# Performance work log

Measured on AMD Instinct MI355X. Metric: run time of the kernel, lower is better.

## Reference

```python
import jax, jax.numpy as jnp
import numpy as np

N, D, H, ED, E, T, L = 100000, 128, 128, 64, 500000, 2, 4


def _ln(x, g, b):
    m = jnp.mean(x, axis=-1, keepdims=True)
    v = jnp.var(x, axis=-1, keepdims=True)
    return (x - m) * jax.lax.rsqrt(v + 1e-5) * g + b


def _seg_softmax(s, seg, n):
    # softmax over edges grouped by segment id (torch scatter-softmax)
    m = jax.ops.segment_max(s, seg, num_segments=n)
    m = jnp.where(jnp.isfinite(m), m, 0.0)
    e = jnp.exp(s - m[seg])
    z = jax.ops.segment_sum(e, seg, num_segments=n)
    return e / (z[seg] + 1e-16)


def setup_inputs() -> dict:
    key = jax.random.key(0)
    ks = iter(jax.random.split(key, 64))
    p = lambda shape: jax.random.normal(next(ks), shape, dtype=jnp.float32) * 0.05
    inp = {
        'node_features': jax.random.normal(next(ks), (N, D), dtype=jnp.float32),
        'edge_features': jax.random.normal(next(ks), (T, E, ED), dtype=jnp.float32),
        'node_levels': jax.random.randint(next(ks), (N,), 0, L, dtype=jnp.int32),
        'edge_index': jax.random.randint(next(ks), (T, 2, E), 0, N, dtype=jnp.int32),
        # NodeLevelAttention params (stacked over T edge types)
        'nl_node_W': p((T, D, H)), 'nl_node_b': p((T, H)),
        'nl_edge_W': p((T, ED, H)), 'nl_edge_b': p((T, H)),
        'nl_att_W1': p((T, 3 * H, H)), 'nl_att_b1': p((T, H)),
        'nl_att_W2': p((T, H, 1)), 'nl_att_b2': p((T, 1)),
        'nl_out_W': p((T, H, H)), 'nl_out_b': p((T, H)),
        'nl_ln_g': jnp.ones((T, H), jnp.float32), 'nl_ln_b': jnp.zeros((T, H), jnp.float32),
        # EdgeLevelAttention params
        'el_att_W1': p((T, H, H)), 'el_att_b1': p((T, H)),
        'el_att_W2': p((T, H, 1)), 'el_att_b2': p((T, 1)),
        'el_out_W': p((H, H)), 'el_out_b': p((H,)),
        'el_ln_g': jnp.ones((H,), jnp.float32), 'el_ln_b': jnp.zeros((H,), jnp.float32),
        # HierarchicalAwarenessModule params
        'hl_proj_W': p((L, H, H)), 'hl_proj_b': p((L, H)),
        'hi_att_W1': p((2 * H, H)), 'hi_att_b1': p((H,)),
        'hi_att_W2': p((H, 1)), 'hi_att_b2': p((1,)),
        'hl_out_W': p((H, H)), 'hl_out_b': p((H,)),
        'hl_ln_g': jnp.ones((H,), jnp.float32), 'hl_ln_b': jnp.zeros((H,), jnp.float32),
    }
    return inp


def reference(node_features, edge_features, node_levels, edge_index,
              nl_node_W, nl_node_b, nl_edge_W, nl_edge_b,
              nl_att_W1, nl_att_b1, nl_att_W2, nl_att_b2,
              nl_out_W, nl_out_b, nl_ln_g, nl_ln_b,
              el_att_W1, el_att_b1, el_att_W2, el_att_b2,
              el_out_W, el_out_b, el_ln_g, el_ln_b,
              hl_proj_W, hl_proj_b, hi_att_W1, hi_att_b1,
              hi_att_W2, hi_att_b2, hl_out_W, hl_out_b, hl_ln_g, hl_ln_b):
    embs, scores = [], []
    for t in range(T):  # small fixed set of edge types
        h = node_features @ nl_node_W[t] + nl_node_b[t]              # [N,H]
        he = edge_features[t] @ nl_edge_W[t] + nl_edge_b[t]          # [E,H]
        s, d = edge_index[t, 0], edge_index[t, 1]
        cat = jnp.concatenate([h[s], h[d], he], axis=-1)             # [E,3H]
        a = jnp.tanh(cat @ nl_att_W1[t] + nl_att_b1[t]) @ nl_att_W2[t] + nl_att_b2[t]
        alpha = _seg_softmax(a[:, 0], s, N)[:, None]                 # softmax over out-edges of src
        agg = jax.ops.segment_sum(alpha * h[d], s, num_segments=N)  # [N,H]
        emb = jax.nn.relu(_ln(agg @ nl_out_W[t] + nl_out_b[t], nl_ln_g[t], nl_ln_b[t]))
        embs.append(emb)
        scores.append(jnp.tanh(emb @ el_att_W1[t] + el_att_b1[t]) @ el_att_W2[t] + el_att_b2[t])
    # EdgeLevelAttention: softmax over edge types per node
    w = jax.nn.softmax(jnp.concatenate(scores, axis=1), axis=1)      # [N,T]
    fused = sum(embs[t] * w[:, t:t + 1] for t in range(T))
    fused = jax.nn.relu(_ln(fused @ el_out_W + el_out_b, el_ln_g, el_ln_b))
    # HierarchicalAwarenessModule (vectorized form of the per-node loop)
    proj_all = jnp.einsum('nd,ldh->lnh', fused, hl_proj_W) + hl_proj_b[:, None, :]
    hf = proj_all[node_levels, jnp.arange(N)]                        # [N,H] level-specific projection
    counts = jax.ops.segment_sum(jnp.ones((N,), fused.dtype), node_levels, num_segments=L)
    lmean = jax.ops.segment_sum(hf, node_levels, num_segments=L) / jnp.maximum(counts, 1.0)[:, None]
    W1a, W1b = hi_att_W1[:H], hi_att_W1[H:]                          # split concat([h_i, mean_l]) matmul
    sc = jnp.tanh((hf @ W1a)[:, None, :] + (lmean @ W1b)[None, :, :] + hi_att_b1) @ hi_att_W2 + hi_att_b2
    aw = jax.nn.softmax(sc[..., 0], axis=1)                          # [N,L]
    enhanced = aw @ lmean                                            # [N,H]
    return jax.nn.relu(_ln(enhanced @ hl_out_W + hl_out_b, hl_ln_g, hl_ln_b))
```

## Files before the change

### kernel.cpp

```cpp
#include <hip/hip_runtime.h>
#include <math.h>

#define NN 100000
#define EE 500000

typedef __attribute__((ext_vector_type(8))) short bf16x8;
typedef __attribute__((ext_vector_type(4))) float f32x4;
#define MFMA __builtin_amdgcn_mfma_f32_16x16x32_bf16

__device__ inline short f2bf(float x) {
    union { float f; unsigned u; } v; v.f = x;
    unsigned r = v.u + 0x7FFF + ((v.u >> 16) & 1);
    return (short)(r >> 16);
}
__device__ inline float bf2f(unsigned short h) {
    union { unsigned u; float f; } v; v.u = ((unsigned)h) << 16; return v.f;
}
__device__ inline float tanhf_fast(float x) {
    float e = __expf(2.0f * x);
    return 1.0f - 2.0f * __builtin_amdgcn_rcpf(e + 1.0f);
}

__device__ inline bf16x8 mk_hi(const float* p) {
    float4 a = *(const float4*)p, b = *(const float4*)(p + 4);
    float v[8] = {a.x, a.y, a.z, a.w, b.x, b.y, b.z, b.w};
    bf16x8 h;
#pragma unroll
    for (int i = 0; i < 8; i++) h[i] = f2bf(v[i]);
    return h;
}
__device__ inline void mk_split(const float* p, bf16x8& hi, bf16x8& lo) {
    float4 a = *(const float4*)p, b = *(const float4*)(p + 4);
    float v[8] = {a.x, a.y, a.z, a.w, b.x, b.y, b.z, b.w};
#pragma unroll
    for (int i = 0; i < 8; i++) {
        short h = f2bf(v[i]);
        hi[i] = h;
        lo[i] = f2bf(v[i] - bf2f((unsigned short)h));
    }
}

__global__ void k_zero(float* __restrict__ p, size_t n) {
    size_t i = (size_t)blockIdx.x * blockDim.x + threadIdx.x;
    size_t stride = (size_t)gridDim.x * blockDim.x;
    for (; i < n; i += stride) p[i] = 0.0f;
}
__global__ void k_zeroi(int* __restrict__ p, int n) {
    int i = blockIdx.x * blockDim.x + threadIdx.x;
    if (i < n) p[i] = 0;
}

__global__ __launch_bounds__(256) void k_hist(const int* __restrict__ eis, int* __restrict__ deg) {
    int e = blockIdx.x * 256 + threadIdx.x;
    if (e < EE) atomicAdd(&deg[eis[e]], 1);
}
__global__ __launch_bounds__(512) void k_scan1(const int* __restrict__ deg,
                                               int* __restrict__ tmp, int* __restrict__ bsum) {
    __shared__ int sh[2][512];
    int b = blockIdx.x, tid = threadIdx.x;
    int i = b * 512 + tid;
    int v = (i < NN) ? deg[i] : 0;
    int cur = 0;
    sh[0][tid] = v;
    __syncthreads();
    for (int off = 1; off < 512; off <<= 1) {
        int nxt = cur ^ 1;
        int a = sh[cur][tid];
        if (tid >= off) a += sh[cur][tid - off];
        sh[nxt][tid] = a;
        __syncthreads();
        cur = nxt;
    }
    int incl = sh[cur][tid];
    if (i < NN) tmp[i] = incl;
    if (tid == 511) bsum[b] = incl;
}
__global__ void k_scan2(const int* __restrict__ bsum, int* __restrict__ boff) {
    __shared__ int sh[2][256];
    int tid = threadIdx.x;
    int v = (tid < 196) ? bsum[tid] : 0;
    int cur = 0;
    sh[0][tid] = v;
    __syncthreads();
    for (int off = 1; off < 256; off <<= 1) {
        int nxt = cur ^ 1;
        int a = sh[cur][tid];
        if (tid >= off) a += sh[cur][tid - off];
        sh[nxt][tid] = a;
        __syncthreads();
        cur = nxt;
    }
    boff[tid] = sh[cur][tid] - v;
}
__global__ __launch_bounds__(512) void k_scan3(const int* __restrict__ deg,
                                               const int* __restrict__ tmp,
                                               const int* __restrict__ boff,
                                               int* __restrict__ rowptr, int* __restrict__ cursor) {
    int i = blockIdx.x * 512 + threadIdx.x;
    if (i < NN) {
        int r = tmp[i] - deg[i] + boff[blockIdx.x];
        rowptr[i] = r;
        cursor[i] = r;
    }
    if (i == 0) rowptr[NN] = EE;
}
__global__ __launch_bounds__(256) void k_csr_scatter(const int* __restrict__ eis,
                                                     const int* __restrict__ eid,
                                                     int* __restrict__ cursor,
                                                     int* __restrict__ epos,
                                                     int* __restrict__ cdst) {
    int e = blockIdx.x * 256 + threadIdx.x;
    if (e < EE) {
        int s = eis[e];
        int p = atomicAdd(&cursor[s], 1);
        epos[e] = p;
        cdst[p] = eid[e];
    }
}

__global__ __launch_bounds__(256) void k_count(const int* __restrict__ lev, int* __restrict__ cnt4) {
    __shared__ int lc[4];
    int tid = threadIdx.x;
    if (tid < 4) lc[tid] = 0;
    __syncthreads();
    for (long n = (long)blockIdx.x * 256 + tid; n < NN; n += (long)gridDim.x * 256)
        atomicAdd(&lc[lev[n]], 1);
    __syncthreads();
    if (tid < 4 && lc[tid]) atomicAdd(&cnt4[tid], lc[tid]);
}

__global__ void k_scan(const int* __restrict__ cnt4, int* __restrict__ off4,
                       int* __restrict__ boff5, int* __restrict__ cursor) {
    int o = 0, b = 0;
    for (int l = 0; l < 4; l++) {
        off4[l] = o; cursor[l] = o; boff5[l] = b;
        o += cnt4[l];
        b += (cnt4[l] + 15) >> 4;
    }
    boff5[4] = b;
}

__global__ __launch_bounds__(256) void k_scatter(const int* __restrict__ lev,
                                                 int* __restrict__ cursor,
                                                 int* __restrict__ perm) {
    __shared__ int lc[4], lb[4], lc2[4];
    int tid = threadIdx.x;
    if (tid < 4) { lc[tid] = 0; lc2[tid] = 0; }
    __syncthreads();
    int start = blockIdx.x * 800, end = start + 800;
    if (end > NN) end = NN;
    for (int n = start + tid; n < end; n += 256) atomicAdd(&lc[lev[n]], 1);
    __syncthreads();
    if (tid < 4 && lc[tid]) lb[tid] = atomicAdd(&cursor[tid], lc[tid]);
    __syncthreads();
    for (int n = start + tid; n < end; n += 256) {
        int l = lev[n];
        int p = atomicAdd(&lc2[l], 1);
        perm[lb[l] + p] = n;
    }
}

__global__ void k_prep_head(const float* __restrict__ Wn, const float* __restrict__ bn,
                            const float* __restrict__ W1, const float* __restrict__ b1,
                            const float* __restrict__ We, const float* __restrict__ be,
                            unsigned short* __restrict__ WhT, unsigned short* __restrict__ WUT,
                            unsigned short* __restrict__ WVT, unsigned short* __restrict__ WET,
                            float* __restrict__ beff) {
    __shared__ float red[2];
    int j = blockIdx.x, k = threadIdx.x;
    WhT[j * 128 + k] = (unsigned short)f2bf(Wn[k * 128 + j]);
    float su = 0.0f, sv = 0.0f;
    for (int m = 0; m < 128; m++) {
        float wkm = Wn[k * 128 + m];
        su = fmaf(wkm, W1[m * 128 + j], su);
        sv = fmaf(wkm, W1[(128 + m) * 128 + j], sv);
    }
    WUT[j * 128 + k] = (unsigned short)f2bf(su);
    WVT[j * 128 + k] = (unsigned short)f2bf(sv);
    if (k < 64) {
        float se = 0.0f;
        for (int m = 0; m < 128; m++) se = fmaf(We[k * 128 + m], W1[(256 + m) * 128 + j], se);
        WET[j * 64 + k] = (unsigned short)f2bf(se);
    }
    float tk = bn[k] * (W1[k * 128 + j] + W1[(128 + k) * 128 + j]) + be[k] * W1[(256 + k) * 128 + j];
#pragma unroll
    for (int o = 32; o > 0; o >>= 1) tk += __shfl_down(tk, o);
    if ((k & 63) == 0) red[k >> 6] = tk;
    __syncthreads();
    if (k == 0) beff[j] = b1[j] + red[0] + red[1];
}

struct WSrc { const float* s[6]; };
__global__ void k_prep_tail(WSrc ps, unsigned short* __restrict__ hi,
                            unsigned short* __restrict__ lo) {
    int m = blockIdx.x >> 6, blk = blockIdx.x & 63;
    const float* src = ps.s[m];
    unsigned short* h = hi + (size_t)m * 16384;
    unsigned short* l = lo + (size_t)m * 16384;
    int idx = blk * 256 + threadIdx.x;
    int k = idx >> 7, j = idx & 127;
    float v = src[idx];
    short hh = f2bf(v);
    h[j * 128 + k] = (unsigned short)hh;
    l[j * 128 + k] = (unsigned short)f2bf(v - bf2f((unsigned short)hh));
}

__global__ void k_prep_q(const float* __restrict__ hpW, const float* __restrict__ hpb,
                         const float* __restrict__ hW1a,
                         unsigned short* __restrict__ QWhi, unsigned short* __restrict__ QWlo,
                         float* __restrict__ qb) {
    int gidx = blockIdx.x * 256 + threadIdx.x;
    if (gidx < 4 * 16384) {
        int l = gidx >> 14, rem = gidx & 16383;
        int k = rem >> 7, j = rem & 127;
        const float* wr = hpW + (size_t)l * 16384 + (size_t)k * 128;
        float v = 0.0f;
        for (int m = 0; m < 128; m++) v = fmaf(wr[m], hW1a[m * 128 + j], v);
        short hh = f2bf(v);
        QWhi[(size_t)l * 16384 + j * 128 + k] = (unsigned short)hh;
        QWlo[(size_t)l * 16384 + j * 128 + k] = (unsigned short)f2bf(v - bf2f((unsigned short)hh));
    } else {
        int e = gidx - 4 * 16384;
        if (e < 512) {
            int l = e >> 7, j = e & 127;
            float v = 0.0f;
            for (int m = 0; m < 128; m++) v = fmaf(hpb[l * 128 + m], hW1a[m * 128 + j], v);
            qb[l * 128 + j] = v;
        }
    }
}

__global__ __launch_bounds__(256) void k_head(const float* __restrict__ nf,
                                              const unsigned short* __restrict__ WhT,
                                              const unsigned short* __restrict__ WUT,
                                              const unsigned short* __restrict__ WVT,
                                              const float* __restrict__ bn,
                                              unsigned short* __restrict__ hbf,
                                              unsigned short* __restrict__ U,
                                              unsigned short* __restrict__ V) {
    __shared__ __align__(16) float T[16][132];
    int tid = threadIdx.x;
    long row0 = (long)blockIdx.x * 16;
#pragma unroll
    for (int i = 0; i < 8; i++) {
        int idx = tid + i * 256;
        int r = idx >> 7, c = idx & 127;
        T[r][c] = nf[(row0 + r) * 128 + c];
    }
    __syncthreads();
    int w = tid >> 6, lane = tid & 63, lr = lane & 15, lg = lane >> 4;
    bf16x8 A[4];
#pragma unroll
    for (int k = 0; k < 4; k++) A[k] = mk_hi(&T[lr][k * 32 + lg * 8]);
    int col0 = w * 32 + lr, col1 = col0 + 16;
#pragma unroll
    for (int o = 0; o < 3; o++) {
        const unsigned short* wb = (o == 0) ? WhT : (o == 1) ? WUT : WVT;
        unsigned short* ob = (o == 0) ? hbf : (o == 1) ? U : V;
        const unsigned short* w0 = wb + (size_t)col0 * 128 + lg * 8;
        const unsigned short* w1 = wb + (size_t)col1 * 128 + lg * 8;
        f32x4 a0 = {0.f, 0.f, 0.f, 0.f}, a1 = {0.f, 0.f, 0.f, 0.f};
#pragma unroll
        for (int k = 0; k < 4; k++) {
            a0 = MFMA(A[k], *(const bf16x8*)(w0 + k * 32), a0, 0, 0, 0);
            a1 = MFMA(A[k], *(const bf16x8*)(w1 + k * 32), a1, 0, 0, 0);
        }
        float bb0 = (o == 0) ? bn[col0] : 0.0f;
        float bb1 = (o == 0) ? bn[col1] : 0.0f;
        unsigned short* op = ob + (size_t)row0 * 128;
#pragma unroll
        for (int i = 0; i < 4; i++) {
            int r = lg * 4 + i;
            op[(size_t)r * 128 + col0] = (unsigned short)f2bf(a0[i] + bb0);
            op[(size_t)r * 128 + col1] = (unsigned short)f2bf(a1[i] + bb1);
        }
    }
}

__global__ __launch_bounds__(256) void k_edge3(const float* __restrict__ ef,
                                               const int* __restrict__ eis,
                                               const int* __restrict__ eid,
                                               const int* __restrict__ epos,
                                               const unsigned short* __restrict__ WET,
                                               const unsigned short* __restrict__ U,
                                               const unsigned short* __restrict__ V,
                                               const float* __restrict__ beff,
                                               const float* __restrict__ W2,
                                               const float* __restrict__ b2p,
                                               float* __restrict__ ebuf) {
    __shared__ __align__(16) float pre[64][132];
    __shared__ float part[4][64];
    int tid = threadIdx.x, w = tid >> 6, lane = tid & 63, lr = lane & 15, lg = lane >> 4;
    long e0 = (long)blockIdx.x * 64;
    long remE = (long)EE - e0;
    int nE = remE < 64 ? (int)remE : 64;
    int n16 = (nE + 15) >> 4;
    {
        int eL = tid >> 2;
        int c4 = tid & 3;
        if (eL < nE) {
            long e = e0 + eL;
            int s = eis[e], d = eid[e];
            const unsigned short* up = U + (size_t)s * 128 + c4 * 32;
            const unsigned short* vp = V + (size_t)d * 128 + c4 * 32;
#pragma unroll
            for (int i = 0; i < 4; i++) {
                bf16x8 uv = *(const bf16x8*)(up + i * 8);
                bf16x8 vv = *(const bf16x8*)(vp + i * 8);
                float4 lo4, hi4;
                lo4.x = bf2f((unsigned short)uv[0]) + bf2f((unsigned short)vv[0]);
                lo4.y = bf2f((unsigned short)uv[1]) + bf2f((unsigned short)vv[1]);
                lo4.z = bf2f((unsigned short)uv[2]) + bf2f((unsigned short)vv[2]);
                lo4.w = bf2f((unsigned short)uv[3]) + bf2f((unsigned short)vv[3]);
                hi4.x = bf2f((unsigned short)uv[4]) + bf2f((unsigned short)vv[4]);
                hi4.y = bf2f((unsigned short)uv[5]) + bf2f((unsigned short)vv[5]);
                hi4.z = bf2f((unsigned short)uv[6]) + bf2f((unsigned short)vv[6]);
                hi4.w = bf2f((unsigned short)uv[7]) + bf2f((unsigned short)vv[7]);
                *(float4*)&pre[eL][c4 * 32 + i * 8] = lo4;
                *(float4*)&pre[eL][c4 * 32 + i * 8 + 4] = hi4;
            }
        }
    }
    int col0 = w * 32 + lr, col1 = col0 + 16;
    bf16x8 B0[2], B1[2];
#pragma unroll
    for (int kk = 0; kk < 2; kk++) {
        B0[kk] = *(const bf16x8*)(WET + (size_t)col0 * 64 + kk * 32 + lg * 8);
        B1[kk] = *(const bf16x8*)(WET + (size_t)col1 * 64 + kk * 32 + lg * 8);
    }
    float be0 = beff[col0], be1 = beff[col1], w20 = W2[col0], w21 = W2[col1];
    __syncthreads();
    for (int i16 = 0; i16 < n16; i16++) {
        long eg0 = e0 + i16 * 16;
        const float* ep = ef + (size_t)(eg0 + lr) * 64;
        f32x4 a0 = {0.f, 0.f, 0.f, 0.f}, a1 = {0.f, 0.f, 0.f, 0.f};
#pragma unroll
        for (int kk = 0; kk < 2; kk++) {
            bf16x8 a = mk_hi(ep + kk * 32 + lg * 8);
            a0 = MFMA(a, B0[kk], a0, 0, 0, 0);
            a1 = MFMA(a, B1[kk], a1, 0, 0, 0);
        }
#pragma unroll
        for (int i = 0; i < 4; i++) {
            int eL = i16 * 16 + lg * 4 + i;
            float v = tanhf_fast(a0[i] + pre[eL][col0] + be0) * w20 +
                      tanhf_fast(a1[i] + pre[eL][col1] + be1) * w21;
            v += __shfl_xor(v, 1);
            v += __shfl_xor(v, 2);
            v += __shfl_xor(v, 4);
            v += __shfl_xor(v, 8);
            if (lr == 0) part[w][eL] = v;
        }
    }
    __syncthreads();
    if (tid < nE) {
        long e = e0 + tid;
        float a = part[0][tid] + part[1][tid] + part[2][tid] + part[3][tid] + b2p[0];
        ebuf[epos[e]] = __expf(a);
    }
}

__global__ __launch_bounds__(256) void k_tailA2(const int* __restrict__ rowptr,
                                                const int* __restrict__ cdst,
                                                const float* __restrict__ ebufC,
                                                const unsigned short* __restrict__ hbf,
                                                const unsigned short* __restrict__ Whi,
                                                const unsigned short* __restrict__ Wlo,
                                                const float* __restrict__ ob,
                                                const float* __restrict__ g,
                                                const float* __restrict__ bln,
                                                const unsigned short* __restrict__ Shi,
                                                const float* __restrict__ sb1,
                                                const float* __restrict__ sW2,
                                                const float* __restrict__ sb2,
                                                float* __restrict__ emb,
                                                float* __restrict__ scores, int t) {
    __shared__ __align__(16) float T[16][132];
    __shared__ __align__(16) float T2[16][132];
    __shared__ float mu16[16], rs16[16], part[4][16];
    int tid = threadIdx.x;
    long row0 = (long)blockIdx.x * 16;
    {
        int r16 = tid >> 4, sub = tid & 15;
        long n = row0 + r16;
        int p0 = rowptr[n], p1 = rowptr[n + 1];
        float acc[8] = {0, 0, 0, 0, 0, 0, 0, 0};
        float sev = 0.0f;
        for (int p = p0; p < p1; p++) {
            int d = cdst[p];
            float ev = ebufC[p];
            bf16x8 hv = *(const bf16x8*)(hbf + (size_t)d * 128 + sub * 8);
            sev += ev;
#pragma unroll
            for (int i = 0; i < 8; i++) acc[i] = fmaf(ev, bf2f((unsigned short)hv[i]), acc[i]);
        }
        float inv = 1.0f / (sev + 1e-16f);
#pragma unroll
        for (int i = 0; i < 8; i++) T[r16][sub * 8 + i] = acc[i] * inv;
    }
    __syncthreads();
    int w = tid >> 6, lane = tid & 63, lr = lane & 15, lg = lane >> 4;
    int col0 = w * 32 + lr, col1 = col0 + 16;
    int j = tid & 127, half = tid >> 7;
    {
        bf16x8 ahi[4], alo[4];
#pragma unroll
        for (int k = 0; k < 4; k++) mk_split(&T[lr][k * 32 + lg * 8], ahi[k], alo[k]);
        const unsigned short* wh0 = Whi + (size_t)col0 * 128 + lg * 8;
        const unsigned short* wl0 = Wlo + (size_t)col0 * 128 + lg * 8;
        const unsigned short* wh1 = Whi + (size_t)col1 * 128 + lg * 8;
        const unsigned short* wl1 = Wlo + (size_t)col1 * 128 + lg * 8;
        f32x4 a0 = {0.f, 0.f, 0.f, 0.f}, a1 = {0.f, 0.f, 0.f, 0.f};
#pragma unroll
        for (int k = 0; k < 4; k++) {
            bf16x8 bh = *(const bf16x8*)(wh0 + k * 32), bl = *(const bf16x8*)(wl0 + k * 32);
            a0 = MFMA(ahi[k], bh, a0, 0, 0, 0);
            a0 = MFMA(alo[k], bh, a0, 0, 0, 0);
            a0 = MFMA(ahi[k], bl, a0, 0, 0, 0);
            bh = *(const bf16x8*)(wh1 + k * 32); bl = *(const bf16x8*)(wl1 + k * 32);
            a1 = MFMA(ahi[k], bh, a1, 0, 0, 0);
            a1 = MFMA(alo[k], bh, a1, 0, 0, 0);
            a1 = MFMA(ahi[k], bl, a1, 0, 0, 0);
        }
#pragma unroll
        for (int i = 0; i < 4; i++) {
            int r = lg * 4 + i;
            T2[r][col0] = a0[i] + ob[col0];
            T2[r][col1] = a1[i] + ob[col1];
        }
    }
    __syncthreads();
    {
        int gr = tid >> 4, l16 = tid & 15;
        float sm = 0.0f, sq = 0.0f;
#pragma unroll
        for (int i = 0; i < 8; i++) {
            float v = T2[gr][l16 + 16 * i];
            sm += v; sq += v * v;
        }
#pragma unroll
        for (int m = 1; m < 16; m <<= 1) { sm += __shfl_xor(sm, m); sq += __shfl_xor(sq, m); }
        if (l16 == 0) {
            float mean = sm * (1.0f / 128.0f);
            float var = sq * (1.0f / 128.0f) - mean * mean;
            mu16[gr] = mean;
            rs16[gr] = rsqrtf(var + 1e-5f);
        }
    }
    __syncthreads();
    {
        float gj = g[j], bb = bln[j];
#pragma unroll
        for (int r = 0; r < 8; r++) {
            int rr = half * 8 + r;
            float v = fmaxf((T2[rr][j] - mu16[rr]) * rs16[rr] * gj + bb, 0.0f);
            emb[(row0 + rr) * 128 + j] = v;
            T2[rr][j] = v;
        }
    }
    __syncthreads();
    {
        bf16x8 ah[4];
#pragma unroll
        for (int k = 0; k < 4; k++) ah[k] = mk_hi(&T2[lr][k * 32 + lg * 8]);
        const unsigned short* wh0 = Shi + (size_t)col0 * 128 + lg * 8;
        const unsigned short* wh1 = Shi + (size_t)col1 * 128 + lg * 8;
        f32x4 a0 = {0.f, 0.f, 0.f, 0.f}, a1 = {0.f, 0.f, 0.f, 0.f};
#pragma unroll
        for (int k = 0; k < 4; k++) {
            a0 = MFMA(ah[k], *(const bf16x8*)(wh0 + k * 32), a0, 0, 0, 0);
            a1 = MFMA(ah[k], *(const bf16x8*)(wh1 + k * 32), a1, 0, 0, 0);
        }
        float b0 = sb1[col0], b1v = sb1[col1], w20 = sW2[col0], w21 = sW2[col1];
#pragma unroll
        for (int i = 0; i < 4; i++) {
            int r = lg * 4 + i;
            float v = tanhf_fast(a0[i] + b0) * w20 + tanhf_fast(a1[i] + b1v) * w21;
            v += __shfl_xor(v, 1);
            v += __shfl_xor(v, 2);
            v += __shfl_xor(v, 4);
            v += __shfl_xor(v, 8);
            if (lr == 0) part[w][r] = v;
        }
    }
    __syncthreads();
    if (tid < 16)
        scores[(row0 + tid) * 2 + t] = part[0][tid] + part[1][tid] + part[2][tid] + part[3][tid] + sb2[0];
}

__global__ __launch_bounds__(256) void k_tailB1(const float* __restrict__ emb0,
                                                const float* __restrict__ emb1,
                                                const float* __restrict__ scores,
                                                const unsigned short* __restrict__ Fhi,
                                                const unsigned short* __restrict__ Flo,
                                                const float* __restrict__ eob,
                                                const float* __restrict__ elg,
                                                const float* __restrict__ elb,
                                                float* __restrict__ fused2) {
    __shared__ __align__(16) float T[16][132];
    __shared__ __align__(16) float T2[16][132];
    __shared__ float mu16[16], rs16[16], w0s[16], w1s[16];
    int tid = threadIdx.x;
    long row0 = (long)blockIdx.x * 16;
    if (tid < 16) {
        long r = row0 + tid;
        float s0 = scores[r * 2], s1 = scores[r * 2 + 1];
        float mx = fmaxf(s0, s1);
        float e0 = __expf(s0 - mx), e1 = __expf(s1 - mx);
        float inv = 1.0f / (e0 + e1);
        w0s[tid] = e0 * inv;
        w1s[tid] = e1 * inv;
    }
    __syncthreads();
#pragma unroll
    for (int i = 0; i < 8; i++) {
        int idx = tid + i * 256;
        int r = idx >> 7, c = idx & 127;
        T[r][c] = w0s[r] * emb0[(row0 + r) * 128 + c] + w1s[r] * emb1[(row0 + r) * 128 + c];
    }
    __syncthreads();
    int w = tid >> 6, lane = tid & 63, lr = lane & 15, lg = lane >> 4;
    int col0 = w * 32 + lr, col1 = col0 + 16;
    int j = tid & 127, half = tid >> 7;
    {
        bf16x8 ahi[4], alo[4];
#pragma unroll
        for (int k = 0; k < 4; k++) mk_split(&T[lr][k * 32 + lg * 8], ahi[k], alo[k]);
        const unsigned short* wh0 = Fhi + (size_t)col0 * 128 + lg * 8;
        const unsigned short* wl0 = Flo + (size_t)col0 * 128 + lg * 8;
        const unsigned short* wh1 = Fhi + (size_t)col1 * 128 + lg * 8;
        const unsigned short* wl1 = Flo + (size_t)col1 * 128 + lg * 8;
        f32x4 a0 = {0.f, 0.f, 0.f, 0.f}, a1 = {0.f, 0.f, 0.f, 0.f};
#pragma unroll
        for (int k = 0; k < 4; k++) {
            bf16x8 bh = *(const bf16x8*)(wh0 + k * 32), bl = *(const bf16x8*)(wl0 + k * 32);
            a0 = MFMA(ahi[k], bh, a0, 0, 0, 0);
            a0 = MFMA(alo[k], bh, a0, 0, 0, 0);
            a0 = MFMA(ahi[k], bl, a0, 0, 0, 0);
            bh = *(const bf16x8*)(wh1 + k * 32); bl = *(const bf16x8*)(wl1 + k * 32);
            a1 = MFMA(ahi[k], bh, a1, 0, 0, 0);
// ... 250 lines not shown
        float gj = hlg[j], bb = hlb[j];
#pragma unroll
        for (int r = 0; r < 8; r++) {
            int rr = half * 8 + r;
            float v = (T2[rr][j] - mu16[rr]) * rs16[rr] * gj + bb;
            out[(size_t)idx16[rr] * 128 + j] = fmaxf(v, 0.0f);
        }
    }
}

extern "C" void kernel_launch(void* const* d_in, const int* in_sizes, int n_in,
                              void* d_out, int out_size, void* d_ws, size_t ws_size,
                              hipStream_t stream) {
    const float* nf  = (const float*)d_in[0];
    const float* ef  = (const float*)d_in[1];
    const int*   lev = (const int*)d_in[2];
    const int*   ei  = (const int*)d_in[3];
    const float* nlW = (const float*)d_in[4];
    const float* nlb = (const float*)d_in[5];
    const float* neW = (const float*)d_in[6];
    const float* neb = (const float*)d_in[7];
    const float* aW1 = (const float*)d_in[8];
    const float* ab1 = (const float*)d_in[9];
    const float* aW2 = (const float*)d_in[10];
    const float* ab2 = (const float*)d_in[11];
    const float* oW  = (const float*)d_in[12];
    const float* ob  = (const float*)d_in[13];
    const float* lng = (const float*)d_in[14];
    const float* lnb = (const float*)d_in[15];
    const float* eW1 = (const float*)d_in[16];
    const float* eb1 = (const float*)d_in[17];
    const float* eW2 = (const float*)d_in[18];
    const float* eb2 = (const float*)d_in[19];
    const float* eoW = (const float*)d_in[20];
    const float* eob = (const float*)d_in[21];
    const float* elg = (const float*)d_in[22];
    const float* elb = (const float*)d_in[23];
    const float* hpW = (const float*)d_in[24];
    const float* hpb = (const float*)d_in[25];
    const float* hW1 = (const float*)d_in[26];
    const float* hb1 = (const float*)d_in[27];
    const float* hW2 = (const float*)d_in[28];
    const float* hb2 = (const float*)d_in[29];
    const float* hoW = (const float*)d_in[30];
    const float* hob = (const float*)d_in[31];
    const float* hlg = (const float*)d_in[32];
    const float* hlb = (const float*)d_in[33];

    float* ws = (float*)d_ws;
    size_t NH = (size_t)NN * 128;
    float* fused2 = ws;
    float* emb0   = fused2 + NH;
    float* emb1   = emb0 + NH;
    float* ebuf   = emb1 + NH;
    float* scores = ebuf + EE;
    float* beff   = scores + (size_t)2 * NN;
    float* fsum   = beff + 128;
    float* lmean  = fsum + 512;
    float* lmw    = lmean + 512;
    float* qb     = lmw + 512;
    unsigned short* U    = (unsigned short*)(qb + 512);
    unsigned short* V    = U + NH;
    unsigned short* hbf  = V + NH;
    unsigned short* WhT  = hbf + NH;
    unsigned short* WUT  = WhT + 16384;
    unsigned short* WVT  = WUT + 16384;
    unsigned short* WET  = WVT + 16384;
    unsigned short* twhi = WET + 8192;
    unsigned short* twlo = twhi + 6 * 16384;
    unsigned short* QWhi = twlo + 6 * 16384;
    unsigned short* QWlo = QWhi + 4 * 16384;
    int* perm  = (int*)(QWlo + 4 * 16384);
    int* cnt4  = perm + NN;
    int* off4  = cnt4 + 4;
    int* boff5 = off4 + 4;
    int* cursorL = boff5 + 5;
    int* epos   = (int*)fused2;
    int* cdst   = epos + EE;
    int* deg    = cdst + EE;
    int* rowptr = deg + NN;
    int* cursor = rowptr + NN + 1;
    int* stmp   = cursor + NN;
    int* sbsum  = stmp + NN;
    int* sboff  = sbsum + 256;
    float* out = (float*)d_out;

    WSrc ps;
    ps.s[0] = oW;
    ps.s[1] = oW + 16384;
    ps.s[2] = eW1;
    ps.s[3] = eW1 + 16384;
    ps.s[4] = eoW;
    ps.s[5] = hoW;

    k_zeroi<<<1, 4, 0, stream>>>(cnt4, 4);
    k_count<<<128, 256, 0, stream>>>(lev, cnt4);
    k_scan<<<1, 1, 0, stream>>>(cnt4, off4, boff5, cursorL);
    k_scatter<<<125, 256, 0, stream>>>(lev, cursorL, perm);

    k_prep_tail<<<6 * 64, 256, 0, stream>>>(ps, twhi, twlo);
    k_prep_q<<<258, 256, 0, stream>>>(hpW, hpb, hW1, QWhi, QWlo, qb);
    k_zero<<<1, 512, 0, stream>>>(fsum, (size_t)512);

    for (int t = 0; t < 2; t++) {
        const int* eis = ei + (size_t)t * 2 * EE;
        const int* eid = eis + EE;
        k_zeroi<<<(NN + 255) / 256, 256, 0, stream>>>(deg, NN);
        k_hist<<<(EE + 255) / 256, 256, 0, stream>>>(eis, deg);
        k_scan1<<<196, 512, 0, stream>>>(deg, stmp, sbsum);
        k_scan2<<<1, 256, 0, stream>>>(sbsum, sboff);
        k_scan3<<<196, 512, 0, stream>>>(deg, stmp, sboff, rowptr, cursor);
        k_csr_scatter<<<(EE + 255) / 256, 256, 0, stream>>>(eis, eid, cursor, epos, cdst);

        k_prep_head<<<128, 128, 0, stream>>>(nlW + (size_t)t * 16384, nlb + t * 128,
                                             aW1 + (size_t)t * 384 * 128, ab1 + t * 128,
                                             neW + (size_t)t * 64 * 128, neb + t * 128,
                                             WhT, WUT, WVT, WET, beff);
        k_head<<<NN / 16, 256, 0, stream>>>(nf, WhT, WUT, WVT, nlb + t * 128, hbf, U, V);
        k_edge3<<<(EE + 63) / 64, 256, 0, stream>>>(ef + (size_t)t * EE * 64, eis, eid, epos,
                                                    WET, U, V, beff, aW2 + t * 128,
                                                    ab2 + t, ebuf);
        float* embt = (t == 0) ? emb0 : emb1;
        k_tailA2<<<NN / 16, 256, 0, stream>>>(rowptr, cdst, ebuf, hbf,
                                              twhi + (size_t)t * 16384, twlo + (size_t)t * 16384,
                                              ob + t * 128, lng + t * 128, lnb + t * 128,
                                              twhi + (size_t)(2 + t) * 16384,
                                              eb1 + t * 128, eW2 + t * 128, eb2 + t,
                                              embt, scores, t);
    }
    k_tailB1<<<NN / 16, 256, 0, stream>>>(emb0, emb1, scores,
                                          twhi + (size_t)4 * 16384, twlo + (size_t)4 * 16384,
                                          eob, elg, elb, fused2);
    k_fsum<<<256, 256, 0, stream>>>(fused2, lev, fsum);
    k_fin2<<<4, 128, 0, stream>>>(fsum, cnt4, hpW, hpb, hW1 + 16384, hb1, lmean, lmw);
    k_tailCD2<<<NN / 16 + 4, 256, 0, stream>>>(fused2, perm, cnt4, off4, boff5,
                                               QWhi, QWlo, qb, lmw, lmean, hW2,
                                               twhi + (size_t)5 * 16384, twlo + (size_t)5 * 16384,
                                               hob, hlg, hlb, out);
}
```

Baseline: 1.041 ms.

## Batch both edge types into single launches for CSR build, head, edge and tail

Merges the per-edge-type loop into single kernels covering both types: one histogram, scan, and CSR scatter over 2N nodes and 2E edges, one prep_head and head kernel producing both types' U/V/h buffers while reading node features once, and doubled grids for the edge and tail kernels. This cuts launch count and serialization and gives larger grids for better GPU fill. The edge kernel also gains a full-tile path that loads features in batches and unrolls the gather loop two edges at a time. The cost is more workspace, since per-type buffers are no longer reused.

```diff
diff --git a/kernel.cpp b/kernel.cpp
--- a/kernel.cpp
+++ b/kernel.cpp
@@ -3,6 +3,7 @@
 
 #define NN 100000
 #define EE 500000
+#define NH_C (NN * 128)
 
 typedef __attribute__((ext_vector_type(8))) short bf16x8;
 typedef __attribute__((ext_vector_type(4))) float f32x4;
@@ -29,6 +30,13 @@
     for (int i = 0; i < 8; i++) h[i] = f2bf(v[i]);
     return h;
 }
+__device__ inline bf16x8 mk_hi8(float4 a, float4 b) {
+    float v[8] = {a.x, a.y, a.z, a.w, b.x, b.y, b.z, b.w};
+    bf16x8 h;
+#pragma unroll
+    for (int i = 0; i < 8; i++) h[i] = f2bf(v[i]);
+    return h;
+}
 __device__ inline void mk_split(const float* p, bf16x8& hi, bf16x8& lo) {
     float4 a = *(const float4*)p, b = *(const float4*)(p + 4);
     float v[8] = {a.x, a.y, a.z, a.w, b.x, b.y, b.z, b.w};
@@ -50,16 +58,21 @@
     if (i < n) p[i] = 0;
 }
 
-__global__ __launch_bounds__(256) void k_hist(const int* __restrict__ eis, int* __restrict__ deg) {
-    int e = blockIdx.x * 256 + threadIdx.x;
-    if (e < EE) atomicAdd(&deg[eis[e]], 1);
+__global__ __launch_bounds__(256) void k_hist2(const int* __restrict__ ei, int* __restrict__ deg2) {
+    long g = (long)blockIdx.x * 256 + threadIdx.x;
+    if (g < 2L * EE) {
+        int t = g >= EE;
+        long le = g - (long)t * EE;
+        int s = ei[(size_t)t * 2 * EE + le];
+        atomicAdd(&deg2[t * NN + s], 1);
+    }
 }
 __global__ __launch_bounds__(512) void k_scan1(const int* __restrict__ deg,
                                                int* __restrict__ tmp, int* __restrict__ bsum) {
     __shared__ int sh[2][512];
     int b = blockIdx.x, tid = threadIdx.x;
     int i = b * 512 + tid;
-    int v = (i < NN) ? deg[i] : 0;
+    int v = (i < 2 * NN) ? deg[i] : 0;
     int cur = 0;
     sh[0][tid] = v;
     __syncthreads();
@@ -72,17 +85,18 @@
         cur = nxt;
     }
     int incl = sh[cur][tid];
-    if (i < NN) tmp[i] = incl;
+    if (i < 2 * NN) tmp[i] = incl;
     if (tid == 511) bsum[b] = incl;
 }
-__global__ void k_scan2(const int* __restrict__ bsum, int* __restrict__ boff) {
-    __shared__ int sh[2][256];
+__global__ __launch_bounds__(512) void k_scan2(const int* __restrict__ bsum, int* __restrict__ boff,
+                                               int nB) {
+    __shared__ int sh[2][512];
     int tid = threadIdx.x;
-    int v = (tid < 196) ? bsum[tid] : 0;
+    int v = (tid < nB) ? bsum[tid] : 0;
     int cur = 0;
     sh[0][tid] = v;
     __syncthreads();
-    for (int off = 1; off < 256; off <<= 1) {
+    for (int off = 1; off < 512; off <<= 1) {
         int nxt = cur ^ 1;
         int a = sh[cur][tid];
         if (tid >= off) a += sh[cur][tid - off];
@@ -97,24 +111,26 @@
                                                const int* __restrict__ boff,
                                                int* __restrict__ rowptr, int* __restrict__ cursor) {
     int i = blockIdx.x * 512 + threadIdx.x;
-    if (i < NN) {
+    if (i < 2 * NN) {
         int r = tmp[i] - deg[i] + boff[blockIdx.x];
         rowptr[i] = r;
         cursor[i] = r;
     }
-    if (i == 0) rowptr[NN] = EE;
-}
-__global__ __launch_bounds__(256) void k_csr_scatter(const int* __restrict__ eis,
-                                                     const int* __restrict__ eid,
-                                                     int* __restrict__ cursor,
-                                                     int* __restrict__ epos,
-                                                     int* __restrict__ cdst) {
-    int e = blockIdx.x * 256 + threadIdx.x;
-    if (e < EE) {
-        int s = eis[e];
-        int p = atomicAdd(&cursor[s], 1);
-        epos[e] = p;
-        cdst[p] = eid[e];
+    if (i == 0) rowptr[2 * NN] = 2 * EE;
+}
+__global__ __launch_bounds__(256) void k_csr_scatter2(const int* __restrict__ ei,
+                                                      int* __restrict__ cursor,
+                                                      int* __restrict__ epos,
+                                                      int* __restrict__ cdst) {
+    long g = (long)blockIdx.x * 256 + threadIdx.x;
+    if (g < 2L * EE) {
+        int t = g >= EE;
+        long le = g - (long)t * EE;
+        int s = ei[(size_t)t * 2 * EE + le];
+        int d = ei[(size_t)t * 2 * EE + EE + le];
+        int p = atomicAdd(&cursor[t * NN + s], 1);
+        epos[g] = p;
+        cdst[p] = d;
     }
 }
 
@@ -160,34 +176,40 @@
     }
 }
 
-__global__ void k_prep_head(const float* __restrict__ Wn, const float* __restrict__ bn,
-                            const float* __restrict__ W1, const float* __restrict__ b1,
-                            const float* __restrict__ We, const float* __restrict__ be,
-                            unsigned short* __restrict__ WhT, unsigned short* __restrict__ WUT,
-                            unsigned short* __restrict__ WVT, unsigned short* __restrict__ WET,
-                            float* __restrict__ beff) {
+__global__ void k_prep_head2(const float* __restrict__ nlW, const float* __restrict__ nlb,
+                             const float* __restrict__ aW1, const float* __restrict__ ab1,
+                             const float* __restrict__ neW, const float* __restrict__ neb,
+                             unsigned short* __restrict__ WhT2, unsigned short* __restrict__ WUT2,
+                             unsigned short* __restrict__ WVT2, unsigned short* __restrict__ WET2,
+                             float* __restrict__ beff2) {
     __shared__ float red[2];
-    int j = blockIdx.x, k = threadIdx.x;
-    WhT[j * 128 + k] = (unsigned short)f2bf(Wn[k * 128 + j]);
+    int t = blockIdx.x >> 7, j = blockIdx.x & 127, k = threadIdx.x;
+    const float* Wn = nlW + (size_t)t * 16384;
+    const float* bn = nlb + t * 128;
+    const float* W1 = aW1 + (size_t)t * 384 * 128;
+    const float* b1 = ab1 + t * 128;
+    const float* We = neW + (size_t)t * 64 * 128;
+    const float* be = neb + t * 128;
+    WhT2[(size_t)t * 16384 + j * 128 + k] = (unsigned short)f2bf(Wn[k * 128 + j]);
     float su = 0.0f, sv = 0.0f;
     for (int m = 0; m < 128; m++) {
         float wkm = Wn[k * 128 + m];
         su = fmaf(wkm, W1[m * 128 + j], su);
         sv = fmaf(wkm, W1[(128 + m) * 128 + j], sv);
     }
-    WUT[j * 128 + k] = (unsigned short)f2bf(su);
-    WVT[j * 128 + k] = (unsigned short)f2bf(sv);
+    WUT2[(size_t)t * 16384 + j * 128 + k] = (unsigned short)f2bf(su);
+    WVT2[(size_t)t * 16384 + j * 128 + k] = (unsigned short)f2bf(sv);
     if (k < 64) {
         float se = 0.0f;
         for (int m = 0; m < 128; m++) se = fmaf(We[k * 128 + m], W1[(256 + m) * 128 + j], se);
-        WET[j * 64 + k] = (unsigned short)f2bf(se);
+        WET2[(size_t)t * 8192 + j * 64 + k] = (unsigned short)f2bf(se);
     }
     float tk = bn[k] * (W1[k * 128 + j] + W1[(128 + k) * 128 + j]) + be[k] * W1[(256 + k) * 128 + j];
 #pragma unroll
     for (int o = 32; o > 0; o >>= 1) tk += __shfl_down(tk, o);
     if ((k & 63) == 0) red[k >> 6] = tk;
     __syncthreads();
-    if (k == 0) beff[j] = b1[j] + red[0] + red[1];
+    if (k == 0) beff2[t * 128 + j] = b1[j] + red[0] + red[1];
 }
 
 struct WSrc { const float* s[6]; };
@@ -230,14 +252,14 @@
     }
 }
 
-__global__ __launch_bounds__(256) void k_head(const float* __restrict__ nf,
-                                              const unsigned short* __restrict__ WhT,
-                                              const unsigned short* __restrict__ WUT,
-                                              const unsigned short* __restrict__ WVT,
-                                              const float* __restrict__ bn,
-                                              unsigned short* __restrict__ hbf,
-                                              unsigned short* __restrict__ U,
-                                              unsigned short* __restrict__ V) {
+__global__ __launch_bounds__(256) void k_head2(const float* __restrict__ nf,
+                                               const unsigned short* __restrict__ WhT2,
+                                               const unsigned short* __restrict__ WUT2,
+                                               const unsigned short* __restrict__ WVT2,
+                                               const float* __restrict__ nlb,
+                                               unsigned short* __restrict__ hbf2,
+                                               unsigned short* __restrict__ U2,
+                                               unsigned short* __restrict__ V2) {
     __shared__ __align__(16) float T[16][132];
     int tid = threadIdx.x;
     long row0 = (long)blockIdx.x * 16;
@@ -254,9 +276,13 @@
     for (int k = 0; k < 4; k++) A[k] = mk_hi(&T[lr][k * 32 + lg * 8]);
     int col0 = w * 32 + lr, col1 = col0 + 16;
 #pragma unroll
-    for (int o = 0; o < 3; o++) {
-        const unsigned short* wb = (o == 0) ? WhT : (o == 1) ? WUT : WVT;
-        unsigned short* ob = (o == 0) ? hbf : (o == 1) ? U : V;
+    for (int o = 0; o < 6; o++) {
+        const unsigned short* wb =
+            (o == 0) ? WhT2 : (o == 1) ? WUT2 : (o == 2) ? WVT2 :
+            (o == 3) ? WhT2 + 16384 : (o == 4) ? WUT2 + 16384 : WVT2 + 16384;
+        unsigned short* ob =
+            (o == 0) ? hbf2 : (o == 1) ? U2 : (o == 2) ? V2 :
+            (o == 3) ? hbf2 + NH_C : (o == 4) ? U2 + NH_C : V2 + NH_C;
         const unsigned short* w0 = wb + (size_t)col0 * 128 + lg * 8;
         const unsigned short* w1 = wb + (size_t)col1 * 128 + lg * 8;
         f32x4 a0 = {0.f, 0.f, 0.f, 0.f}, a1 = {0.f, 0.f, 0.f, 0.f};
@@ -265,8 +291,8 @@
             a0 = MFMA(A[k], *(const bf16x8*)(w0 + k * 32), a0, 0, 0, 0);
             a1 = MFMA(A[k], *(const bf16x8*)(w1 + k * 32), a1, 0, 0, 0);
         }
-        float bb0 = (o == 0) ? bn[col0] : 0.0f;
-        float bb1 = (o == 0) ? bn[col1] : 0.0f;
+        float bb0 = (o == 0) ? nlb[col0] : (o == 3) ? nlb[128 + col0] : 0.0f;
+        float bb1 = (o == 0) ? nlb[col1] : (o == 3) ? nlb[128 + col1] : 0.0f;
         unsigned short* op = ob + (size_t)row0 * 128;
 #pragma unroll
         for (int i = 0; i < 4; i++) {
@@ -277,32 +303,38 @@
     }
 }
 
-__global__ __launch_bounds__(256) void k_edge3(const float* __restrict__ ef,
-                                               const int* __restrict__ eis,
-                                               const int* __restrict__ eid,
-                                               const int* __restrict__ epos,
-                                               const unsigned short* __restrict__ WET,
-                                               const unsigned short* __restrict__ U,
-                                               const unsigned short* __restrict__ V,
-                                               const float* __restrict__ beff,
-                                               const float* __restrict__ W2,
-                                               const float* __restrict__ b2p,
-                                               float* __restrict__ ebuf) {
+__global__ __launch_bounds__(256) void k_edge3b(const float* __restrict__ ef,
+                                                const int* __restrict__ ei,
+                                                const int* __restrict__ epos2,
+                                                const unsigned short* __restrict__ WET2,
+                                                const unsigned short* __restrict__ U2,
+                                                const unsigned short* __restrict__ V2,
+                                                const float* __restrict__ beff2,
+                                                const float* __restrict__ aW2,
+                                                const float* __restrict__ ab2,
+                                                float* __restrict__ ebuf2, int NB) {
     __shared__ __align__(16) float pre[64][132];
     __shared__ float part[4][64];
     int tid = threadIdx.x, w = tid >> 6, lane = tid & 63, lr = lane & 15, lg = lane >> 4;
-    long e0 = (long)blockIdx.x * 64;
+    int t = blockIdx.x >= NB;
+    int bi = blockIdx.x - t * NB;
+    long e0 = (long)bi * 64;
     long remE = (long)EE - e0;
     int nE = remE < 64 ? (int)remE : 64;
-    int n16 = (nE + 15) >> 4;
+    const float* ef_t = ef + (size_t)t * EE * 64;
+    const int* eis = ei + (size_t)t * 2 * EE;
+    const int* eid = eis + EE;
+    const int* eposT = epos2 + (size_t)t * EE;
+    const unsigned short* U_t = U2 + (size_t)t * NH_C;
+    const unsigned short* V_t = V2 + (size_t)t * NH_C;
     {
         int eL = tid >> 2;
         int c4 = tid & 3;
         if (eL < nE) {
             long e = e0 + eL;
             int s = eis[e], d = eid[e];
-            const unsigned short* up = U + (size_t)s * 128 + c4 * 32;
-            const unsigned short* vp = V + (size_t)d * 128 + c4 * 32;
+            const unsigned short* up = U_t + (size_t)s * 128 + c4 * 32;
+            const unsigned short* vp = V_t + (size_t)d * 128 + c4 * 32;
 #pragma unroll
             for (int i = 0; i < 4; i++) {
                 bf16x8 uv = *(const bf16x8*)(up + i * 8);
@@ -325,71 +357,136 @@
     bf16x8 B0[2], B1[2];
 #pragma unroll
     for (int kk = 0; kk < 2; kk++) {
-        B0[kk] = *(const bf16x8*)(WET + (size_t)col0 * 64 + kk * 32 + lg * 8);
-        B1[kk] = *(const bf16x8*)(WET + (size_t)col1 * 64 + kk * 32 + lg * 8);
-    }
-    float be0 = beff[col0], be1 = beff[col1], w20 = W2[col0], w21 = W2[col1];
-    __syncthreads();
-    for (int i16 = 0; i16 < n16; i16++) {
-        long eg0 = e0 + i16 * 16;
-        const float* ep = ef + (size_t)(eg0 + lr) * 64;
-        f32x4 a0 = {0.f, 0.f, 0.f, 0.f}, a1 = {0.f, 0.f, 0.f, 0.f};
-#pragma unroll
-        for (int kk = 0; kk < 2; kk++) {
-            bf16x8 a = mk_hi(ep + kk * 32 + lg * 8);
-            a0 = MFMA(a, B0[kk], a0, 0, 0, 0);
-            a1 = MFMA(a, B1[kk], a1, 0, 0, 0);
-        }
-#pragma unroll
-        for (int i = 0; i < 4; i++) {
-            int eL = i16 * 16 + lg * 4 + i;
-            float v = tanhf_fast(a0[i] + pre[eL][col0] + be0) * w20 +
-                      tanhf_fast(a1[i] + pre[eL][col1] + be1) * w21;
-            v += __shfl_xor(v, 1);
-            v += __shfl_xor(v, 2);
-            v += __shfl_xor(v, 4);
-            v += __shfl_xor(v, 8);
-            if (lr == 0) part[w][eL] = v;
+        B0[kk] = *(const bf16x8*)(WET2 + (size_t)t * 8192 + (size_t)col0 * 64 + kk * 32 + lg * 8);
+        B1[kk] = *(const bf16x8*)(WET2 + (size_t)t * 8192 + (size_t)col1 * 64 + kk * 32 + lg * 8);
+    }
+    float be0 = beff2[t * 128 + col0], be1 = beff2[t * 128 + col1];
+    float w20 = aW2[t * 128 + col0], w21 = aW2[t * 128 + col1];
+    __syncthreads();
+    if (nE == 64) {
+#pragma unroll
+        for (int h2 = 0; h2 < 2; h2++) {
+            float4 L[8];
+#pragma unroll
+            for (int i = 0; i < 2; i++) {
+                const float* ep = ef_t + (size_t)(e0 + (h2 * 2 + i) * 16 + lr) * 64 + lg * 8;
+                L[i * 4 + 0] = *(const float4*)ep;
+                L[i * 4 + 1] = *(const float4*)(ep + 4);
+                L[i * 4 + 2] = *(const float4*)(ep + 32);
+                L[i * 4 + 3] = *(const float4*)(ep + 36);
+            }
+#pragma unroll
+            for (int i = 0; i < 2; i++) {
+                int i16 = h2 * 2 + i;
+                bf16x8 av0 = mk_hi8(L[i * 4 + 0], L[i * 4 + 1]);
+                bf16x8 av1 = mk_hi8(L[i * 4 + 2], L[i * 4 + 3]);
+                f32x4 a0 = {0.f, 0.f, 0.f, 0.f}, a1 = {0.f, 0.f, 0.f, 0.f};
+                a0 = MFMA(av0, B0[0], a0, 0, 0, 0);
+                a0 = MFMA(av1, B0[1], a0, 0, 0, 0);
+                a1 = MFMA(av0, B1[0], a1, 0, 0, 0);
+                a1 = MFMA(av1, B1[1], a1, 0, 0, 0);
+#pragma unroll
+                for (int q = 0; q < 4; q++) {
+                    int eL = i16 * 16 + lg * 4 + q;
+                    float v = tanhf_fast(a0[q] + pre[eL][col0] + be0) * w20 +
+                              tanhf_fast(a1[q] + pre[eL][col1] + be1) * w21;
+                    v += __shfl_xor(v, 1);
+                    v += __shfl_xor(v, 2);
+                    v += __shfl_xor(v, 4);
+                    v += __shfl_xor(v, 8);
+                    if (lr == 0) part[w][eL] = v;
+                }
+            }
+        }
+    } else {
+        int n16 = (nE + 15) >> 4;
+        for (int i16 = 0; i16 < n16; i16++) {
+            long eg0 = e0 + i16 * 16;
+            const float* ep = ef_t + (size_t)(eg0 + lr) * 64;
+            f32x4 a0 = {0.f, 0.f, 0.f, 0.f}, a1 = {0.f, 0.f, 0.f, 0.f};
+#pragma unroll
+            for (int kk = 0; kk < 2; kk++) {
+                bf16x8 a = mk_hi(ep + kk * 32 + lg * 8);
+                a0 = MFMA(a, B0[kk], a0, 0, 0, 0);
+                a1 = MFMA(a, B1[kk], a1, 0, 0, 0);
+            }
+#pragma unroll
+            for (int q = 0; q < 4; q++) {
+                int eL = i16 * 16 + lg * 4 + q;
+                float v = tanhf_fast(a0[q] + pre[eL][col0] + be0) * w20 +
+                          tanhf_fast(a1[q] + pre[eL][col1] + be1) * w21;
+                v += __shfl_xor(v, 1);
+                v += __shfl_xor(v, 2);
+                v += __shfl_xor(v, 4);
+                v += __shfl_xor(v, 8);
+                if (lr == 0) part[w][eL] = v;
+            }
         }
     }
     __syncthreads();
     if (tid < nE) {
         long e = e0 + tid;
-        float a = part[0][tid] + part[1][tid] + part[2][tid] + part[3][tid] + b2p[0];
-        ebuf[epos[e]] = __expf(a);
-    }
-}
-
-__global__ __launch_bounds__(256) void k_tailA2(const int* __restrict__ rowptr,
-                                                const int* __restrict__ cdst,
-                                                const float* __restrict__ ebufC,
-                                                const unsigned short* __restrict__ hbf,
-                                                const unsigned short* __restrict__ Whi,
-                                                const unsigned short* __restrict__ Wlo,
-                                                const float* __restrict__ ob,
-                                                const float* __restrict__ g,
-                                                const float* __restrict__ bln,
-                                                const unsigned short* __restrict__ Shi,
-                                                const float* __restrict__ sb1,
-                                                const float* __restrict__ sW2,
-                                                const float* __restrict__ sb2,
-                                                float* __restrict__ emb,
-                                                float* __restrict__ scores, int t) {
+        float a = part[0][tid] + part[1][tid] + part[2][tid] + part[3][tid] + ab2[t];
+        ebuf2[eposT[e]] = __expf(a);
+    }
+}
+
+__global__ __launch_bounds__(256) void k_tailA2b(const int* __restrict__ rowptr2,
+                                                 const int* __restrict__ cdst,
+                                                 const float* __restrict__ ebufC,
+                                                 const unsigned short* __restrict__ hbf2,
+                                                 const unsigned short* __restrict__ twhi,
+                                                 const unsigned short* __restrict__ twlo,
+                                                 const float* __restrict__ ob,
+                                                 const float* __restrict__ lng,
+                                                 const float* __restrict__ lnb,
+                                                 const float* __restrict__ eb1,
+                                                 const float* __restrict__ eW2,
+                                                 const float* __restrict__ eb2,
+                                                 float* __restrict__ emb0,
+                                                 float* __restrict__ emb1,
+                                                 float* __restrict__ scores, int NBn) {
     __shared__ __align__(16) float T[16][132];
     __shared__ __align__(16) float T2[16][132];
     __shared__ float mu16[16], rs16[16], part[4][16];
     int tid = threadIdx.x;
-    long row0 = (long)blockIdx.x * 16;
+    int t = blockIdx.x >= NBn;
+    int bi = blockIdx.x - t * NBn;
+    long row0 = (long)bi * 16;
+    const int* rowp = rowptr2 + (size_t)t * NN;
+    const unsigned short* hbf_t = hbf2 + (size_t)t * NH_C;
+    const unsigned short* Whi = twhi + (size_t)t * 16384;
+    const unsigned short* Wlo = twlo + (size_t)t * 16384;
+    const unsigned short* Shi = twhi + (size_t)(2 + t) * 16384;
+    const float* ob_t = ob + t * 128;
+    const float* g_t = lng + t * 128;
+    const float* bln_t = lnb + t * 128;
+    const float* sb1 = eb1 + t * 128;
+    const float* sW2 = eW2 + t * 128;
+    float* emb = t ? emb1 : emb0;
     {
         int r16 = tid >> 4, sub = tid & 15;
         long n = row0 + r16;
-        int p0 = rowptr[n], p1 = rowptr[n + 1];
+        int p0 = rowp[n], p1 = rowp[n + 1];
         float acc[8] = {0, 0, 0, 0, 0, 0, 0, 0};
         float sev = 0.0f;
-        for (int p = p0; p < p1; p++) {
+        int p = p0;
+        for (; p + 2 <= p1; p += 2) {
+            int d0 = cdst[p], d1 = cdst[p + 1];
+            float ev0 = ebufC[p], ev1 = ebufC[p + 1];
+            bf16x8 h0 = *(const bf16x8*)(hbf_t + (size_t)d0 * 128 + sub * 8);
+            bf16x8 h1 = *(const bf16x8*)(hbf_t + (size_t)d1 * 128 + sub * 8);
+            sev += ev0 + ev1;
+#pragma unroll
+            for (int i = 0; i < 8; i++) {
+                acc[i] = fmaf(ev0, bf2f((unsigned short)h0[i]), acc[i]);
+                acc[i] = fmaf(ev1, bf2f((unsigned short)h1[i]), acc[i]);
+            }
+        }
+        if (p < p1) {
             int d = cdst[p];
             float ev = ebufC[p];
-            bf16x8 hv = *(const bf16x8*)(hbf + (size_t)d * 128 + sub * 8);
+            bf16x8 hv = *(const bf16x8*)(hbf_t + (size_t)d * 128 + sub * 8);
             sev += ev;
 #pragma unroll
             for (int i = 0; i < 8; i++) acc[i] = fmaf(ev, bf2f((unsigned short)hv[i]), acc[i]);
@@ -425,8 +522,8 @@
 #pragma unroll
         for (int i = 0; i < 4; i++) {
             int r = lg * 4 + i;
-            T2[r][col0] = a0[i] + ob[col0];
-            T2[r][col1] = a1[i] + ob[col1];
+            T2[r][col0] = a0[i] + ob_t[col0];
+            T2[r][col1] = a1[i] + ob_t[col1];
         }
     }
     __syncthreads();
@@ -449,7 +546,7 @@
     }
     __syncthreads();
     {
-        float gj = g[j], bb = bln[j];
+        float gj = g_t[j], bb = bln_t[j];
 #pragma unroll
         for (int r = 0; r < 8; r++) {
             int rr = half * 8 + r;
@@ -485,7 +582,7 @@
     }
     __syncthreads();
     if (tid < 16)
-        scores[(row0 + tid) * 2 + t] = part[0][tid] + part[1][tid] + part[2][tid] + part[3][tid] + sb2[0];
+        scores[(row0 + tid) * 2 + t] = part[0][tid] + part[1][tid] + part[2][tid] + part[3][tid] + eb2[t];
 }
 
 __global__ __launch_bounds__(256) void k_tailB1(const float* __restrict__ emb0,
@@ -842,37 +939,37 @@
     float* fused2 = ws;
     float* emb0   = fused2 + NH;
     float* emb1   = emb0 + NH;
-    float* ebuf   = emb1 + NH;
-    float* scores = ebuf + EE;
-    float* beff   = scores + (size_t)2 * NN;
-    float* fsum   = beff + 128;
+    float* ebuf2  = emb1 + NH;
+    float* scores = ebuf2 + 2 * (size_t)EE;
+    float* beff2  = scores + (size_t)2 * NN;
+    float* fsum   = beff2 + 256;
     float* lmean  = fsum + 512;
     float* lmw    = lmean + 512;
     float* qb     = lmw + 512;
-    unsigned short* U    = (unsigned short*)(qb + 512);
-    unsigned short* V    = U + NH;
-    unsigned short* hbf  = V + NH;
-    unsigned short* WhT  = hbf + NH;
-    unsigned short* WUT  = WhT + 16384;
-    unsigned short* WVT  = WUT + 16384;
-    unsigned short* WET  = WVT + 16384;
-    unsigned short* twhi = WET + 8192;
-    unsigned short* twlo = twhi + 6 * 16384;
-    unsigned short* QWhi = twlo + 6 * 16384;
-    unsigned short* QWlo = QWhi + 4 * 16384;
-    int* perm  = (int*)(QWlo + 4 * 16384);
-    int* cnt4  = perm + NN;
-    int* off4  = cnt4 + 4;
-    int* boff5 = off4 + 4;
+    unsigned short* U2    = (unsigned short*)(qb + 512);
+    unsigned short* V2    = U2 + 2 * NH;
+    unsigned short* hbf2  = V2 + 2 * NH;
+    unsigned short* WhT2  = hbf2 + 2 * NH;
+    unsigned short* WUT2  = WhT2 + 2 * 16384;
+    unsigned short* WVT2  = WUT2 + 2 * 16384;
+    unsigned short* WET2  = WVT2 + 2 * 16384;
+    unsigned short* twhi  = WET2 + 2 * 8192;
+    unsigned short* twlo  = twhi + 6 * 16384;
+    unsigned short* QWhi  = twlo + 6 * 16384;
+    unsigned short* QWlo  = QWhi + 4 * 16384;
+    int* perm    = (int*)(QWlo + 4 * 16384);
+    int* cnt4    = perm + NN;
+    int* off4    = cnt4 + 4;
+    int* boff5   = off4 + 4;
     int* cursorL = boff5 + 5;
-    int* epos   = (int*)fused2;
-    int* cdst   = epos + EE;
-    int* deg    = cdst + EE;
-    int* rowptr = deg + NN;
-    int* cursor = rowptr + NN + 1;
-    int* stmp   = cursor + NN;
-    int* sbsum  = stmp + NN;
-    int* sboff  = sbsum + 256;
+    int* deg2    = cursorL + 4;
+    int* rowptr2 = deg2 + 2 * NN;
+    int* cursor2 = rowptr2 + 2 * NN + 1;
+    int* stmp    = cursor2 + 2 * NN;
+    int* sbsum   = stmp + 2 * NN;
+    int* sboff   = sbsum + 512;
+    int* epos2   = sboff + 512;
+    int* cdst2   = epos2 + 2 * EE;
     float* out = (float*)d_out;
 
     WSrc ps;
@@ -883,6 +980,10 @@
     ps.s[4] = eoW;
     ps.s[5] = hoW;
 
+    const int NB_E = (EE + 63) / 64;
+    const int NB_N = NN / 16;
+    const int SCB = (2 * NN + 511) / 512;
+
     k_zeroi<<<1, 4, 0, stream>>>(cnt4, 4);
     k_count<<<128, 256, 0, stream>>>(lev, cnt4);
     k_scan<<<1, 1, 0, stream>>>(cnt4, off4, boff5, cursorL);
@@ -892,39 +993,30 @@
     k_prep_q<<<258, 256, 0, stream>>>(hpW, hpb, hW1, QWhi, QWlo, qb);
     k_zero<<<1, 512, 0, stream>>>(fsum, (size_t)512);
 
-    for (int t = 0; t < 2; t++) {
-        const int* eis = ei + (size_t)t * 2 * EE;
-        const int* eid = eis + EE;
-        k_zeroi<<<(NN + 255) / 256, 256, 0, stream>>>(deg, NN);
-        k_hist<<<(EE + 255) / 256, 256, 0, stream>>>(eis, deg);
-        k_scan1<<<196, 512, 0, stream>>>(deg, stmp, sbsum);
-        k_scan2<<<1, 256, 0, stream>>>(sbsum, sboff);
-        k_scan3<<<196, 512, 0, stream>>>(deg, stmp, sboff, rowptr, cursor);
-        k_csr_scatter<<<(EE + 255) / 256, 256, 0, stream>>>(eis, eid, cursor, epos, cdst);
-
-        k_prep_head<<<128, 128, 0, stream>>>(nlW + (size_t)t * 16384, nlb + t * 128,
-                                             aW1 + (size_t)t * 384 * 128, ab1 + t * 128,
-                                             neW + (size_t)t * 64 * 128, neb + t * 128,
-                                             WhT, WUT, WVT, WET, beff);
-        k_head<<<NN / 16, 256, 0, stream>>>(nf, WhT, WUT, WVT, nlb + t * 128, hbf, U, V);
-        k_edge3<<<(EE + 63) / 64, 256, 0, stream>>>(ef + (size_t)t * EE * 64, eis, eid, epos,
-                                                    WET, U, V, beff, aW2 + t * 128,
-                                                    ab2 + t, ebuf);
-        float* embt = (t == 0) ? emb0 : emb1;
-        k_tailA2<<<NN / 16, 256, 0, stream>>>(rowptr, cdst, ebuf, hbf,
-                                              twhi + (size_t)t * 16384, twlo + (size_t)t * 16384,
-                                              ob + t * 128, lng + t * 128, lnb + t * 128,
-                                              twhi + (size_t)(2 + t) * 16384,
-                                              eb1 + t * 128, eW2 + t * 128, eb2 + t,
-                                              embt, scores, t);
-    }
-    k_tailB1<<<NN / 16, 256, 0, stream>>>(emb0, emb1, scores,
-                                          twhi + (size_t)4 * 16384, twlo + (size_t)4 * 16384,
-                                          eob, elg, elb, fused2);
+    k_zeroi<<<(2 * NN + 255) / 256, 256, 0, stream>>>(deg2, 2 * NN);
+    k_hist2<<<(2 * EE + 255) / 256, 256, 0, stream>>>(ei, deg2);
+    k_scan1<<<SCB, 512, 0, stream>>>(deg2, stmp, sbsum);
+    k_scan2<<<1, 512, 0, stream>>>(sbsum, sboff, SCB);
+    k_scan3<<<SCB, 512, 0, stream>>>(deg2, stmp, sboff, rowptr2, cursor2);
+    k_csr_scatter2<<<(2 * EE + 255) / 256, 256, 0, stream>>>(ei, cursor2, epos2, cdst2);
+
+    k_prep_head2<<<256, 128, 0, stream>>>(nlW, nlb, aW1, ab1, neW, neb,
+                                          WhT2, WUT2, WVT2, WET2, beff2);
+    k_head2<<<NB_N, 256, 0, stream>>>(nf, WhT2, WUT2, WVT2, nlb, hbf2, U2, V2);
+
+    k_edge3b<<<2 * NB_E, 256, 0, stream>>>(ef, ei, epos2, WET2, U2, V2, beff2,
+                                           aW2, ab2, ebuf2, NB_E);
+    k_tailA2b<<<2 * NB_N, 256, 0, stream>>>(rowptr2, cdst2, ebuf2, hbf2, twhi, twlo,
+                                            ob, lng, lnb, eb1, eW2, eb2,
+                                            emb0, emb1, scores, NB_N);
+
+    k_tailB1<<<NB_N, 256, 0, stream>>>(emb0, emb1, scores,
+                                       twhi + (size_t)4 * 16384, twlo + (size_t)4 * 16384,
+                                       eob, elg, elb, fused2);
     k_fsum<<<256, 256, 0, stream>>>(fused2, lev, fsum);
     k_fin2<<<4, 128, 0, stream>>>(fsum, cnt4, hpW, hpb, hW1 + 16384, hb1, lmean, lmw);
-    k_tailCD2<<<NN / 16 + 4, 256, 0, stream>>>(fused2, perm, cnt4, off4, boff5,
-                                               QWhi, QWlo, qb, lmw, lmean, hW2,
-                                               twhi + (size_t)5 * 16384, twlo + (size_t)5 * 16384,
-                                               hob, hlg, hlb, out);
-}
+    k_tailCD2<<<NB_N + 4, 256, 0, stream>>>(fused2, perm, cnt4, off4, boff5,
+                                            QWhi, QWlo, qb, lmw, lmean, hW2,
+                                            twhi + (size_t)5 * 16384, twlo + (size_t)5 * 16384,
+                                            hob, hlg, hlb, out);
+}
```

Result: faster. 962.1 us (-7.6%).
